# Performance work log

Hardware: AMD Instinct MI355X
Metric: run time of the kernel (lower is better)

## Reference

```python
import jax, jax.numpy as jnp
import numpy as np

B, T, N, F_OUT, K, HID = 8, 12, 4096, 12, 3, 64
HALF = T // 2


def setup_inputs() -> dict:
    key = jax.random.key(0)
    ks = jax.random.split(key, 7)
    return {
        "x": jax.random.normal(ks[0], (B, T, N, 1), jnp.float32),
        "adj": jax.random.normal(ks[1], (K, N, N), jnp.float32) / np.float32(np.sqrt(N)),
        "cheb_w": jax.random.normal(ks[2], (HID, K), jnp.float32) / np.float32(np.sqrt(K)),
        "gcn_w": jax.random.normal(ks[3], (F_OUT, T, 1, HID), jnp.float32) / np.float32(np.sqrt(T * HID)),
        "gcn_b": jnp.zeros((F_OUT,), jnp.float32),
        "glu1_w": jax.random.normal(ks[4], (F_OUT, HALF, 3, 3), jnp.float32) / np.float32(np.sqrt(HALF * 9)),
        "glu1_b": jnp.zeros((F_OUT,), jnp.float32),
        "glu2_w": jax.random.normal(ks[5], (F_OUT, HALF, 3, 3), jnp.float32) / np.float32(np.sqrt(HALF * 9)),
        "glu2_b": jnp.zeros((F_OUT,), jnp.float32),
    }


def _dilated_conv(x, w, b):
    # Conv2d(kernel=3, dilation=2, padding=2) on (B, C, N, 1)
    y = jax.lax.conv_general_dilated(
        x, w, window_strides=(1, 1), padding=((2, 2), (2, 2)),
        rhs_dilation=(2, 2), dimension_numbers=("NCHW", "OIHW", "NCHW"))
    return y + b[None, :, None, None]


def reference(x, adj, cheb_w, gcn_w, gcn_b, glu1_w, glu1_b, glu2_w, glu2_b):
    # --- ChebConv (vectorized over the per-channel Python loop) ---
    # x: (B, T, N, 1), adj: (K, N, N) -> y: (B, T, N, K)
    y = jnp.einsum("knm,btm->btnk", adj, x[..., 0])
    # Linear(K -> HID, no bias) + ReLU -> cheb: (B, T, N, HID)
    cheb = jax.nn.relu(jnp.einsum("btnk,ok->btno", y, cheb_w))
    # --- gcn_conv: Conv2d(T -> F_OUT, kernel (1, HID)) -> (B, F_OUT, N, 1) ---
    sgc = jnp.einsum("btnj,otj->bon", cheb, gcn_w[:, :, 0, :]) + gcn_b[None, :, None]
    sgc = sgc[..., None]
    # --- GLU path: split history in half, dilated convs, a * sigmoid(g) ---
    x_u, x_v = x[:, :HALF], x[:, HALF:]
    a = _dilated_conv(x_u, glu1_w, glu1_b)
    g = _dilated_conv(x_v, glu2_w, glu2_b)
    x_glu = a * jax.nn.sigmoid(g)
    return x_glu + sgc
```

## Files before the change

### kernel.cpp

```cpp
#include <hip/hip_runtime.h>
#include <hip/hip_bf16.h>
#include <math.h>

#define NNODES 4096
#define NCOLS  96
#define NROWS  12288
#define BM     48
#define BK     64

typedef __attribute__((ext_vector_type(8))) short short8;
typedef __attribute__((ext_vector_type(4))) float float4v;

__global__ void probe_dtype(const unsigned int* __restrict__ aw, int* __restrict__ flag) {
    int tid = threadIdx.x;
    unsigned w = aw[tid];
    unsigned e = (w >> 7) & 0xffu;
    bool insane = (e >= 0xC0u) || (e <= 0x30u);
    unsigned long long m = __ballot(insane);
    if (tid == 0) flag[0] = (__popcll(m) >= 16) ? 1 : 0;
}

__device__ __forceinline__ float ldf(const void* p, size_t i, int isf32) {
    return isf32 ? ((const float*)p)[i]
                 : __bfloat162float(((const __hip_bfloat16*)p)[i]);
}

__device__ __forceinline__ void ld8(float* d, const void* p, size_t e, int isf32) {
    if (isf32) {
        const float4* s = (const float4*)((const float*)p + e);
        float4 f0 = s[0], f1 = s[1];
        d[0] = f0.x; d[1] = f0.y; d[2] = f0.z; d[3] = f0.w;
        d[4] = f1.x; d[5] = f1.y; d[6] = f1.z; d[7] = f1.w;
    } else {
        const __hip_bfloat16* s = (const __hip_bfloat16*)p + e;
#pragma unroll
        for (int j = 0; j < 8; j++) d[j] = __bfloat162float(s[j]);
    }
}

__device__ __forceinline__ short8 cvt8(float4 a, float4 b) {
    union { short8 v; __hip_bfloat16 h[8]; } u;
    u.h[0] = __float2bfloat16(a.x); u.h[1] = __float2bfloat16(a.y);
    u.h[2] = __float2bfloat16(a.z); u.h[3] = __float2bfloat16(a.w);
    u.h[4] = __float2bfloat16(b.x); u.h[5] = __float2bfloat16(b.y);
    u.h[6] = __float2bfloat16(b.z); u.h[7] = __float2bfloat16(b.w);
    return u.v;
}

__global__ __launch_bounds__(192) void gemm_y(
    const void* __restrict__ adjv, const void* __restrict__ xv,
    float* __restrict__ yws, const int* __restrict__ flag)
{
    __shared__ __align__(16) short8 As[2][BM * 8];
    __shared__ __align__(16) short8 Xs[2][96 * 8];

    const int tid = threadIdx.x;
    const int isf32 = flag[0];
    const size_t row0 = (size_t)blockIdx.x * BM;

    const int wv = tid >> 6;
    const int ln = tid & 63;
    const int fr = ln & 15;
    const int fq = ln >> 4;

    float4v acc[6];
#pragma unroll
    for (int i = 0; i < 6; i++) acc[i] = (float4v){0.f, 0.f, 0.f, 0.f};

    int arow[2], acol[2], aslot[2];
#pragma unroll
    for (int s = 0; s < 2; s++) {
        int g = tid + s * 192;
        arow[s] = g >> 3; acol[s] = (g & 7) * 8;
        aslot[s] = (g >> 3) * 8 + ((g & 7) ^ ((g >> 3) & 7));
    }
    int xrow[4], xcol[4], xslot[4];
#pragma unroll
    for (int s = 0; s < 4; s++) {
        int g = tid + s * 192;
        xrow[s] = g >> 3; xcol[s] = (g & 7) * 8;
        xslot[s] = (g >> 3) * 8 + ((g & 7) ^ ((g >> 3) & 7));
    }

    if (isf32) {
        const float* adjf = (const float*)adjv;
        const float* xf   = (const float*)xv;

        float4 pa[2][2], px[4][2];
#pragma unroll
        for (int s = 0; s < 2; s++) {
            const float* p = adjf + (row0 + arow[s]) * NNODES + acol[s];
            pa[s][0] = *(const float4*)p; pa[s][1] = *(const float4*)(p + 4);
        }
#pragma unroll
        for (int s = 0; s < 4; s++) {
            const float* p = xf + (size_t)xrow[s] * NNODES + xcol[s];
            px[s][0] = *(const float4*)p; px[s][1] = *(const float4*)(p + 4);
        }

        int buf = 0;
        for (int kk = 0; kk < NNODES; kk += BK) {
#pragma unroll
            for (int s = 0; s < 2; s++) As[buf][aslot[s]] = cvt8(pa[s][0], pa[s][1]);
#pragma unroll
            for (int s = 0; s < 4; s++) Xs[buf][xslot[s]] = cvt8(px[s][0], px[s][1]);
            if (kk + BK < NNODES) {
                const int kn = kk + BK;
#pragma unroll
                for (int s = 0; s < 2; s++) {
                    const float* p = adjf + (row0 + arow[s]) * NNODES + kn + acol[s];
                    pa[s][0] = *(const float4*)p; pa[s][1] = *(const float4*)(p + 4);
                }
#pragma unroll
                for (int s = 0; s < 4; s++) {
                    const float* p = xf + (size_t)xrow[s] * NNODES + kn + xcol[s];
                    px[s][0] = *(const float4*)p; px[s][1] = *(const float4*)(p + 4);
                }
            }
            __syncthreads();
#pragma unroll
            for (int kq = 0; kq < 2; kq++) {
                short8 a = As[buf][(wv * 16 + fr) * 8 + ((kq * 4 + fq) ^ (fr & 7))];
#pragma unroll
                for (int ct = 0; ct < 6; ct++) {
                    short8 bfr = Xs[buf][(ct * 16 + fr) * 8 + ((kq * 4 + fq) ^ (fr & 7))];
                    acc[ct] = __builtin_amdgcn_mfma_f32_16x16x32_bf16(a, bfr, acc[ct], 0, 0, 0);
                }
            }
            buf ^= 1;
        }
    } else {
        const __hip_bfloat16* adjb = (const __hip_bfloat16*)adjv;
        const __hip_bfloat16* xb   = (const __hip_bfloat16*)xv;

        uint4 pa[2], px[4];
#pragma unroll
        for (int s = 0; s < 2; s++)
            pa[s] = *(const uint4*)(adjb + (row0 + arow[s]) * NNODES + acol[s]);
#pragma unroll
        for (int s = 0; s < 4; s++)
            px[s] = *(const uint4*)(xb + (size_t)xrow[s] * NNODES + xcol[s]);

        int buf = 0;
        for (int kk = 0; kk < NNODES; kk += BK) {
#pragma unroll
            for (int s = 0; s < 2; s++) *(uint4*)&As[buf][aslot[s]] = pa[s];
#pragma unroll
            for (int s = 0; s < 4; s++) *(uint4*)&Xs[buf][xslot[s]] = px[s];
            if (kk + BK < NNODES) {
                const int kn = kk + BK;
#pragma unroll
                for (int s = 0; s < 2; s++)
                    pa[s] = *(const uint4*)(adjb + (row0 + arow[s]) * NNODES + kn + acol[s]);
#pragma unroll
                for (int s = 0; s < 4; s++)
                    px[s] = *(const uint4*)(xb + (size_t)xrow[s] * NNODES + kn + xcol[s]);
            }
            __syncthreads();
#pragma unroll
            for (int kq = 0; kq < 2; kq++) {
                short8 a = As[buf][(wv * 16 + fr) * 8 + ((kq * 4 + fq) ^ (fr & 7))];
#pragma unroll
                for (int ct = 0; ct < 6; ct++) {
                    short8 bfr = Xs[buf][(ct * 16 + fr) * 8 + ((kq * 4 + fq) ^ (fr & 7))];
                    acc[ct] = __builtin_amdgcn_mfma_f32_16x16x32_bf16(a, bfr, acc[ct], 0, 0, 0);
                }
            }
            buf ^= 1;
        }
    }

#pragma unroll
    for (int ct = 0; ct < 6; ct++)
#pragma unroll
        for (int rg = 0; rg < 4; rg++) {
            size_t r = row0 + wv * 16 + fq * 4 + rg;
            yws[r * NCOLS + ct * 16 + fr] = acc[ct][rg];
        }
}

__global__ __launch_bounds__(256) void epilogue_kernel(
    const void* __restrict__ xv, const float* __restrict__ yws,
    const void* __restrict__ chebv, const void* __restrict__ gcnwv,
    const void* __restrict__ gcnbv, const void* __restrict__ g1wv,
    const void* __restrict__ g1bv, const void* __restrict__ g2wv,
    const void* __restrict__ g2bv,
    float* __restrict__ out, const int* __restrict__ flag)
{
    __shared__ float gwL[9216];
    __shared__ float cwL[192];
    __shared__ float w1L[216];
    __shared__ float w2L[216];
    __shared__ float wbL[36];

    const int tid = threadIdx.x;
    const int isf32 = flag[0];

    for (int i = tid; i < 9216; i += 256) {
        int o = i / 768, t = (i / 64) % 12, j = i % 64;
        gwL[t * 768 + j * 12 + o] = ldf(gcnwv, i, isf32);
    }
    if (tid < 192) cwL[tid] = ldf(chebv, tid, isf32);
    if (tid < 216) {
        w1L[tid] = ldf(g1wv, (size_t)tid * 3 + 1, isf32);
        w2L[tid] = ldf(g2wv, (size_t)tid * 3 + 1, isf32);
    }
    if (tid < 12) {
        wbL[tid]      = ldf(gcnbv, tid, isf32);
        wbL[12 + tid] = ldf(g1bv, tid, isf32);
        wbL[24 + tid] = ldf(g2bv, tid, isf32);
    }
    __syncthreads();

    const int gid = blockIdx.x * 256 + tid;
    const int pr  = gid >> 2;
    const int tq  = gid & 3;
    const int b = pr >> 12;
    const int n = pr & (NNODES - 1);

    float yk[3][3];
#pragma unroll
    for (int k = 0; k < 3; k++) {
        const float* yp = yws + ((size_t)(k * NNODES + n)) * NCOLS + b * 12 + tq * 3;
        yk[k][0] = yp[0]; yk[k][1] = yp[1]; yk[k][2] = yp[2];
    }

    float sg[12];
#pragma unroll
    for (int o = 0; o < 12; o++) sg[o] = 0.f;
#pragma unroll
    for (int i = 0; i < 3; i++) {
        const float y0 = yk[0][i], y1 = yk[1][i], y2 = yk[2][i];
        const float* gwt = gwL + (tq * 3 + i) * 768;
#pragma unroll 4
        for (int j = 0; j < 64; j++) {
            float h = y0 * cwL[j * 3] + y1 * cwL[j * 3 + 1] + y2 * cwL[j * 3 + 2];
            h = fmaxf(h, 0.f);
#pragma unroll
            for (int o = 0; o < 12; o++) sg[o] += h * gwt[j * 12 + o];
        }
    }
#pragma unroll
    for (int o = 0; o < 12; o++) {
        sg[o] += __shfl_xor(sg[o], 1);
        sg[o] += __shfl_xor(sg[o], 2);
    }

    float xa[18], xg[18];
#pragma unroll
    for (int c = 0; c < 6; c++)
#pragma unroll
        for (int kh = 0; kh < 3; kh++) {
            int m = n + 2 * kh - 2;
            bool ok = ((unsigned)m < (unsigned)NNODES);
            xa[c * 3 + kh] = ok ? ldf(xv, ((size_t)(b * 12 + c)) * NNODES + m, isf32) : 0.f;
            xg[c * 3 + kh] = ok ? ldf(xv, ((size_t)(b * 12 + c + 6)) * NNODES + m, isf32) : 0.f;
        }

#pragma unroll
    for (int i = 0; i < 3; i++) {
        const int o = tq * 3 + i;
        float av = wbL[12 + o], gv = wbL[24 + o];
#pragma unroll
        for (int q = 0; q < 18; q++) {
            av += xa[q] * w1L[o * 18 + q];
            gv += xg[q] * w2L[o * 18 + q];
        }
        float s = 1.f / (1.f + expf(-gv));
        out[((size_t)(b * 12 + o)) * NNODES + n] = av * s + sg[o] + wbL[o];
    }
}

__global__ __launch_bounds__(64) void fused_simple(
    const void* __restrict__ xv, const void* __restrict__ adjv,
    const void* __restrict__ chebv, const void* __restrict__ gcnwv,
    const void* __restrict__ gcnbv, const void* __restrict__ g1wv,
    const void* __restrict__ g1bv, const void* __restrict__ g2wv,
    const void* __restrict__ g2bv,
    float* __restrict__ out, const int* __restrict__ flag)
{
    __shared__ float gwL[9216];
    __shared__ float cwL[192];
    __shared__ float w1L[216];
    __shared__ float w2L[216];
    __shared__ float wbL[36];

    const int tid = threadIdx.x;
    const int isf32 = flag[0];

    for (int i = tid; i < 9216; i += 64) {
        int o = i / 768, t = (i / 64) % 12, j = i % 64;
        gwL[t * 768 + j * 12 + o] = ldf(gcnwv, i, isf32);
    }
    for (int i = tid; i < 192; i += 64) cwL[i] = ldf(chebv, i, isf32);
    for (int i = tid; i < 216; i += 64) {
        w1L[i] = ldf(g1wv, (size_t)i * 3 + 1, isf32);
        w2L[i] = ldf(g2wv, (size_t)i * 3 + 1, isf32);
    }
    if (tid < 12) {
        wbL[tid]      = ldf(gcnbv, tid, isf32);
        wbL[12 + tid] = ldf(g1bv, tid, isf32);
        wbL[24 + tid] = ldf(g2bv, tid, isf32);
    }
    __syncthreads();

    const int g = blockIdx.x * 64 + tid;
    const int b = g >> 12;
    const int n = g & (NNODES - 1);

    float y[3][12];
#pragma unroll
    for (int k = 0; k < 3; k++)
#pragma unroll
        for (int t = 0; t < 12; t++) y[k][t] = 0.f;

    for (int m0 = 0; m0 < NNODES; m0 += 8) {
        float a0[8], a1[8], a2[8];
        ld8(a0, adjv, ((size_t)(0 * NNODES + n)) * NNODES + m0, isf32);
        ld8(a1, adjv, ((size_t)(1 * NNODES + n)) * NNODES + m0, isf32);
        ld8(a2, adjv, ((size_t)(2 * NNODES + n)) * NNODES + m0, isf32);
#pragma unroll
        for (int t = 0; t < 12; t++) {
            float x8[8];
            ld8(x8, xv, ((size_t)(b * 12 + t)) * NNODES + m0, isf32);
#pragma unroll
            for (int j = 0; j < 8; j++) {
                y[0][t] += a0[j] * x8[j];
                y[1][t] += a1[j] * x8[j];
                y[2][t] += a2[j] * x8[j];
            }
        }
    }

    float sg[12];
#pragma unroll
    for (int o = 0; o < 12; o++) sg[o] = wbL[o];
    for (int t = 0; t < 12; t++) {
        const float y0 = y[0][t], y1 = y[1][t], y2 = y[2][t];
        const float* gwt = gwL + t * 768;
#pragma unroll 4
        for (int j = 0; j < 64; j++) {
            float h = y0 * cwL[j * 3] + y1 * cwL[j * 3 + 1] + y2 * cwL[j * 3 + 2];
            h = fmaxf(h, 0.f);
#pragma unroll
            for (int o = 0; o < 12; o++) sg[o] += h * gwt[j * 12 + o];
        }
    }

    float xa[18], xg[18];
#pragma unroll
    for (int c = 0; c < 6; c++)
#pragma unroll
        for (int kh = 0; kh < 3; kh++) {
            int m = n + 2 * kh - 2;
            bool ok = ((unsigned)m < (unsigned)NNODES);
            xa[c * 3 + kh] = ok ? ldf(xv, ((size_t)(b * 12 + c)) * NNODES + m, isf32) : 0.f;
            xg[c * 3 + kh] = ok ? ldf(xv, ((size_t)(b * 12 + c + 6)) * NNODES + m, isf32) : 0.f;
        }

#pragma unroll
    for (int o = 0; o < 12; o++) {
        float av = wbL[12 + o], gv = wbL[24 + o];
#pragma unroll
        for (int i = 0; i < 18; i++) {
            av += xa[i] * w1L[o * 18 + i];
            gv += xg[i] * w2L[o * 18 + i];
        }
        float s = 1.f / (1.f + expf(-gv));
        out[((size_t)(b * 12 + o)) * NNODES + n] = av * s + sg[o];
    }
}

extern "C" void kernel_launch(void* const* d_in, const int* in_sizes, int n_in,
                              void* d_out, int out_size, void* d_ws, size_t ws_size,
                              hipStream_t stream)
{
    int* flag = (int*)d_ws;
    float* yws = (float*)((char*)d_ws + 64);
    const size_t need = 64 + (size_t)NROWS * NCOLS * 4;

    hipLaunchKernelGGL(probe_dtype, dim3(1), dim3(64), 0, stream,
                       (const unsigned int*)d_in[1], flag);

    if (ws_size >= need) {
        hipLaunchKernelGGL(gemm_y, dim3(256), dim3(192), 0, stream,
                           d_in[1], d_in[0], yws, flag);
        hipLaunchKernelGGL(epilogue_kernel, dim3(512), dim3(256), 0, stream,
                           d_in[0], yws, d_in[2], d_in[3], d_in[4],
                           d_in[5], d_in[6], d_in[7], d_in[8],
                           (float*)d_out, flag);
    } else {
        hipLaunchKernelGGL(fused_simple, dim3(512), dim3(64), 0, stream,
                           d_in[0], d_in[1], d_in[2], d_in[3], d_in[4],
                           d_in[5], d_in[6], d_in[7], d_in[8],
                           (float*)d_out, flag);
    }
}
```

Before: 367.6 us.

## Split GEMM K dimension across waves and load fragments directly from global

Rewrites gemm_y so that each wave independently computes a 16-row tile over one quarter of the K range. MFMA fragments are loaded straight from global memory into registers with double buffering, with no shared memory and no block barriers. The launch grows from 256 to 768 blocks for more parallelism, and the epilogue sums four partial Y buffers. The cost is a workspace four times larger plus extra partial-sum traffic. The per-lane global loads are strided by row rather than coalesced, and the x operand is re-read by every wave.

```diff
diff --git a/kernel.cpp b/kernel.cpp
--- a/kernel.cpp
+++ b/kernel.cpp
@@ -5,8 +5,8 @@
 #define NNODES 4096
 #define NCOLS  96
 #define NROWS  12288
-#define BM     48
-#define BK     64
+#define KSEG   4
+#define KLEN   (NNODES / KSEG)
 
 typedef __attribute__((ext_vector_type(8))) short short8;
 typedef __attribute__((ext_vector_type(4))) float float4v;
@@ -47,135 +47,103 @@
     return u.v;
 }
 
-__global__ __launch_bounds__(192) void gemm_y(
+__global__ __launch_bounds__(256) void gemm_y(
     const void* __restrict__ adjv, const void* __restrict__ xv,
     float* __restrict__ yws, const int* __restrict__ flag)
 {
-    __shared__ __align__(16) short8 As[2][BM * 8];
-    __shared__ __align__(16) short8 Xs[2][96 * 8];
-
     const int tid = threadIdx.x;
     const int isf32 = flag[0];
-    const size_t row0 = (size_t)blockIdx.x * BM;
-
     const int wv = tid >> 6;
     const int ln = tid & 63;
     const int fr = ln & 15;
     const int fq = ln >> 4;
 
+    const int gw = blockIdx.x * 4 + wv;
+    const int rt = gw >> 2;
+    const int ks = gw & 3;
+    const int k0 = ks * KLEN;
+
     float4v acc[6];
 #pragma unroll
     for (int i = 0; i < 6; i++) acc[i] = (float4v){0.f, 0.f, 0.f, 0.f};
-
-    int arow[2], acol[2], aslot[2];
-#pragma unroll
-    for (int s = 0; s < 2; s++) {
-        int g = tid + s * 192;
-        arow[s] = g >> 3; acol[s] = (g & 7) * 8;
-        aslot[s] = (g >> 3) * 8 + ((g & 7) ^ ((g >> 3) & 7));
-    }
-    int xrow[4], xcol[4], xslot[4];
-#pragma unroll
-    for (int s = 0; s < 4; s++) {
-        int g = tid + s * 192;
-        xrow[s] = g >> 3; xcol[s] = (g & 7) * 8;
-        xslot[s] = (g >> 3) * 8 + ((g & 7) ^ ((g >> 3) & 7));
-    }
 
     if (isf32) {
         const float* adjf = (const float*)adjv;
         const float* xf   = (const float*)xv;
-
-        float4 pa[2][2], px[4][2];
-#pragma unroll
-        for (int s = 0; s < 2; s++) {
-            const float* p = adjf + (row0 + arow[s]) * NNODES + acol[s];
-            pa[s][0] = *(const float4*)p; pa[s][1] = *(const float4*)(p + 4);
-        }
-#pragma unroll
-        for (int s = 0; s < 4; s++) {
-            const float* p = xf + (size_t)xrow[s] * NNODES + xcol[s];
-            px[s][0] = *(const float4*)p; px[s][1] = *(const float4*)(p + 4);
-        }
-
-        int buf = 0;
-        for (int kk = 0; kk < NNODES; kk += BK) {
-#pragma unroll
-            for (int s = 0; s < 2; s++) As[buf][aslot[s]] = cvt8(pa[s][0], pa[s][1]);
-#pragma unroll
-            for (int s = 0; s < 4; s++) Xs[buf][xslot[s]] = cvt8(px[s][0], px[s][1]);
-            if (kk + BK < NNODES) {
-                const int kn = kk + BK;
-#pragma unroll
-                for (int s = 0; s < 2; s++) {
-                    const float* p = adjf + (row0 + arow[s]) * NNODES + kn + acol[s];
-                    pa[s][0] = *(const float4*)p; pa[s][1] = *(const float4*)(p + 4);
-                }
-#pragma unroll
-                for (int s = 0; s < 4; s++) {
-                    const float* p = xf + (size_t)xrow[s] * NNODES + kn + xcol[s];
-                    px[s][0] = *(const float4*)p; px[s][1] = *(const float4*)(p + 4);
-                }
-            }
-            __syncthreads();
-#pragma unroll
-            for (int kq = 0; kq < 2; kq++) {
-                short8 a = As[buf][(wv * 16 + fr) * 8 + ((kq * 4 + fq) ^ (fr & 7))];
-#pragma unroll
-                for (int ct = 0; ct < 6; ct++) {
-                    short8 bfr = Xs[buf][(ct * 16 + fr) * 8 + ((kq * 4 + fq) ^ (fr & 7))];
-                    acc[ct] = __builtin_amdgcn_mfma_f32_16x16x32_bf16(a, bfr, acc[ct], 0, 0, 0);
-                }
-            }
-            buf ^= 1;
-        }
+        const float* aptr = adjf + (size_t)(rt * 16 + fr) * NNODES + k0 + fq * 8;
+        const float* xptr[6];
+#pragma unroll
+        for (int ct = 0; ct < 6; ct++)
+            xptr[ct] = xf + (size_t)(ct * 16 + fr) * NNODES + k0 + fq * 8;
+
+        float4 raA[2], rxA[6][2], raB[2], rxB[6][2];
+
+#define LOADF(RA, RX, KB) {                                                   \
+        { const float* p = aptr + (KB);                                       \
+          RA[0] = *(const float4*)p; RA[1] = *(const float4*)(p + 4); }       \
+        _Pragma("unroll")                                                     \
+        for (int ct = 0; ct < 6; ct++) {                                      \
+            const float* p = xptr[ct] + (KB);                                 \
+            RX[ct][0] = *(const float4*)p; RX[ct][1] = *(const float4*)(p + 4);\
+        } }
+#define COMPF(RA, RX) {                                                       \
+        short8 a = cvt8(RA[0], RA[1]);                                        \
+        _Pragma("unroll")                                                     \
+        for (int ct = 0; ct < 6; ct++) {                                      \
+            short8 b = cvt8(RX[ct][0], RX[ct][1]);                            \
+            acc[ct] = __builtin_amdgcn_mfma_f32_16x16x32_bf16(a, b, acc[ct], 0, 0, 0); \
+        } }
+
+        LOADF(raA, rxA, 0);
+        for (int it = 0; it < KLEN / 32; it += 2) {
+            LOADF(raB, rxB, (it + 1) * 32);
+            COMPF(raA, rxA);
+            if (it + 2 < KLEN / 32) LOADF(raA, rxA, (it + 2) * 32);
+            COMPF(raB, rxB);
+        }
+#undef LOADF
+#undef COMPF
     } else {
         const __hip_bfloat16* adjb = (const __hip_bfloat16*)adjv;
         const __hip_bfloat16* xb   = (const __hip_bfloat16*)xv;
-
-        uint4 pa[2], px[4];
-#pragma unroll
-        for (int s = 0; s < 2; s++)
-            pa[s] = *(const uint4*)(adjb + (row0 + arow[s]) * NNODES + acol[s]);
-#pragma unroll
-        for (int s = 0; s < 4; s++)
-            px[s] = *(const uint4*)(xb + (size_t)xrow[s] * NNODES + xcol[s]);
-
-        int buf = 0;
-        for (int kk = 0; kk < NNODES; kk += BK) {
-#pragma unroll
-            for (int s = 0; s < 2; s++) *(uint4*)&As[buf][aslot[s]] = pa[s];
-#pragma unroll
-            for (int s = 0; s < 4; s++) *(uint4*)&Xs[buf][xslot[s]] = px[s];
-            if (kk + BK < NNODES) {
-                const int kn = kk + BK;
-#pragma unroll
-                for (int s = 0; s < 2; s++)
-                    pa[s] = *(const uint4*)(adjb + (row0 + arow[s]) * NNODES + kn + acol[s]);
-#pragma unroll
-                for (int s = 0; s < 4; s++)
-                    px[s] = *(const uint4*)(xb + (size_t)xrow[s] * NNODES + kn + xcol[s]);
-            }
-            __syncthreads();
-#pragma unroll
-            for (int kq = 0; kq < 2; kq++) {
-                short8 a = As[buf][(wv * 16 + fr) * 8 + ((kq * 4 + fq) ^ (fr & 7))];
-#pragma unroll
-                for (int ct = 0; ct < 6; ct++) {
-                    short8 bfr = Xs[buf][(ct * 16 + fr) * 8 + ((kq * 4 + fq) ^ (fr & 7))];
-                    acc[ct] = __builtin_amdgcn_mfma_f32_16x16x32_bf16(a, bfr, acc[ct], 0, 0, 0);
-                }
-            }
-            buf ^= 1;
-        }
-    }
-
+        const __hip_bfloat16* aptr = adjb + (size_t)(rt * 16 + fr) * NNODES + k0 + fq * 8;
+        const __hip_bfloat16* xptr[6];
+#pragma unroll
+        for (int ct = 0; ct < 6; ct++)
+            xptr[ct] = xb + (size_t)(ct * 16 + fr) * NNODES + k0 + fq * 8;
+
+        uint4 raA, rxA[6], raB, rxB[6];
+
+#define LOADB(RA, RX, KB) {                                                   \
+        RA = *(const uint4*)(aptr + (KB));                                    \
+        _Pragma("unroll")                                                     \
+        for (int ct = 0; ct < 6; ct++) RX[ct] = *(const uint4*)(xptr[ct] + (KB)); }
+#define COMPB(RA, RX) {                                                       \
+        short8 a = *(const short8*)&RA;                                       \
+        _Pragma("unroll")                                                     \
+        for (int ct = 0; ct < 6; ct++) {                                      \
+            short8 b = *(const short8*)&RX[ct];                               \
+            acc[ct] = __builtin_amdgcn_mfma_f32_16x16x32_bf16(a, b, acc[ct], 0, 0, 0); \
+        } }
+
+        LOADB(raA, rxA, 0);
+        for (int it = 0; it < KLEN / 32; it += 2) {
+            LOADB(raB, rxB, (it + 1) * 32);
+            COMPB(raA, rxA);
+            if (it + 2 < KLEN / 32) LOADB(raA, rxA, (it + 2) * 32);
+            COMPB(raB, rxB);
+        }
+#undef LOADB
+#undef COMPB
+    }
+
+    float* yo = yws + (size_t)ks * NROWS * NCOLS;
 #pragma unroll
     for (int ct = 0; ct < 6; ct++)
 #pragma unroll
         for (int rg = 0; rg < 4; rg++) {
-            size_t r = row0 + wv * 16 + fq * 4 + rg;
-            yws[r * NCOLS + ct * 16 + fr] = acc[ct][rg];
+            size_t r = (size_t)rt * 16 + fq * 4 + rg;
+            yo[r * NCOLS + ct * 16 + fr] = acc[ct][rg];
         }
 }
 
@@ -220,9 +188,15 @@
 
     float yk[3][3];
 #pragma unroll
-    for (int k = 0; k < 3; k++) {
-        const float* yp = yws + ((size_t)(k * NNODES + n)) * NCOLS + b * 12 + tq * 3;
-        yk[k][0] = yp[0]; yk[k][1] = yp[1]; yk[k][2] = yp[2];
+    for (int k = 0; k < 3; k++) { yk[k][0] = 0.f; yk[k][1] = 0.f; yk[k][2] = 0.f; }
+#pragma unroll
+    for (int s = 0; s < KSEG; s++) {
+        const float* base = yws + (size_t)s * NROWS * NCOLS;
+#pragma unroll
+        for (int k = 0; k < 3; k++) {
+            const float* yp = base + ((size_t)(k * NNODES + n)) * NCOLS + b * 12 + tq * 3;
+            yk[k][0] += yp[0]; yk[k][1] += yp[1]; yk[k][2] += yp[2];
+        }
     }
 
     float sg[12];
@@ -377,13 +351,13 @@
 {
     int* flag = (int*)d_ws;
     float* yws = (float*)((char*)d_ws + 64);
-    const size_t need = 64 + (size_t)NROWS * NCOLS * 4;
+    const size_t need = 64 + (size_t)KSEG * NROWS * NCOLS * 4;
 
     hipLaunchKernelGGL(probe_dtype, dim3(1), dim3(64), 0, stream,
                        (const unsigned int*)d_in[1], flag);
 
     if (ws_size >= need) {
-        hipLaunchKernelGGL(gemm_y, dim3(256), dim3(192), 0, stream,
+        hipLaunchKernelGGL(gemm_y, dim3(768), dim3(256), 0, stream,
                            d_in[1], d_in[0], yws, flag);
         hipLaunchKernelGGL(epilogue_kernel, dim3(512), dim3(256), 0, stream,
                            d_in[0], yws, d_in[2], d_in[3], d_in[4],
```

New measurement: 439.2 us. +19.5%, slower.
